# Optimization experiments

Hardware: AMD Instinct MI355X
Metric: run time of the kernel (lower is better)

## Reference

```python
import jax, jax.numpy as jnp
import numpy as np

B, L = 256, 50            # batch, n_pos (session length)
ITEM_DIM, POS_DIM = 128, 64
DIM = ITEM_DIM + POS_DIM  # 192
N_ITEMS = 50000
W = 20.0                  # temperature / init scale
LN_EPS = 1e-5


def renorm(t, max_norm=1.5):
    # torch Embedding max_norm semantics: clip row L2 norm to max_norm
    n = jnp.linalg.norm(t, axis=-1, keepdims=True)
    return t * jnp.minimum(1.0, max_norm / jnp.maximum(n, 1e-7))


def setup_inputs() -> dict:
    key = jax.random.key(0)
    ks = jax.random.split(key, 24)
    inv_w = 1.0 / W
    lb = 1.0 / np.sqrt(DIM)
    lb3 = 1.0 / np.sqrt(3 * DIM)
    u = lambda k, shape, b: jax.random.uniform(k, shape, jnp.float32, -b, b)
    emb = jax.random.normal(ks[0], (N_ITEMS, ITEM_DIM), jnp.float32).at[0].set(0.0)
    pos_emb = jax.random.normal(ks[1], (L + 1, POS_DIM), jnp.float32).at[0].set(0.0)
    return {
        'x': jax.random.randint(ks[20], (B, L), 0, N_ITEMS),
        'pos': jnp.sort(jax.random.randint(ks[21], (B, L), 1, L + 1), axis=-1),
        'emb': emb,
        'pos_emb': pos_emb,
        'vw0': jax.random.normal(ks[2], (1, DIM), jnp.float32) * inv_w,
        'vw1': jax.random.normal(ks[3], (DIM, DIM), jnp.float32) * inv_w,
        'vw2': jax.random.normal(ks[4], (DIM, DIM), jnp.float32) * inv_w,
        'vbias': jnp.zeros((DIM,), jnp.float32),
        'w1_W': u(ks[5], (DIM, DIM), lb), 'w1_b': u(ks[6], (DIM,), lb),
        'w2_W': u(ks[7], (DIM, DIM), lb), 'w2_b': u(ks[8], (DIM,), lb),
        'wA': jax.random.normal(ks[9], (1, L), jnp.float32) * inv_w,
        'wg1_W': u(ks[10], (DIM, DIM), lb), 'wg1_b': u(ks[11], (DIM,), lb),
        'wg2_W': u(ks[12], (DIM, DIM), lb), 'wg2_b': u(ks[13], (DIM,), lb),
        'gq': jax.random.normal(ks[14], (DIM, 1), jnp.float32) * inv_w,
        'wf_W': u(ks[15], (ITEM_DIM, 3 * DIM), lb3), 'wf_b': u(ks[16], (ITEM_DIM,), lb3),
        'ln_g': jnp.ones((DIM,), jnp.float32), 'ln_b': jnp.zeros((DIM,), jnp.float32),
    }


def reference(x, pos, emb, pos_emb, vw0, vw1, vw2, vbias, w1_W, w1_b, w2_W, w2_b,
              wA, wg1_W, wg1_b, wg2_W, wg2_b, gq, wf_W, wf_b, ln_g, ln_b):
    emb_r = renorm(emb)
    x_e = emb_r[x]                                   # [B,L,item_dim]
    p_e = renorm(pos_emb)[pos]                       # [B,L,pos_dim]
    x_ = jnp.concatenate([x_e, p_e], axis=-1)        # [B,L,D]
    mask = (x != 0)                                  # [B,L]

    # --- vanila (additive) attention, all n_pos targets in one fused pass ---
    K = x_ @ vw1                                     # [B,L,D]  (shared across targets)
    Q = x_ @ vw2                                     # [B,L,D]
    h = jax.nn.relu(K[:, None, :, :] + Q[:, :, None, :] + vbias)   # [B,Li,Lj,D]
    alpha = jnp.einsum('bijd,d->bij', h, vw0[0])     # scores over keys j
    alpha = jnp.where(mask[:, None, :], alpha, -jnp.inf)
    a = jax.nn.softmax(alpha, axis=-1)
    S = jnp.einsum('bij,bjd->bid', a, x_)            # [B,L,D]

    # --- MLP + LayerNorm + position mixing ---
    h2 = jax.nn.relu(S @ w1_W.T + w1_b)
    S2 = h2 @ w2_W.T + w2_b + S
    mu = jnp.mean(S2, axis=-1, keepdims=True)
    var = jnp.mean((S2 - mu) ** 2, axis=-1, keepdims=True)
    S3 = ln_g * (S2 - mu) * jax.lax.rsqrt(var + LN_EPS) + ln_b
    st = jnp.einsum('p,bpd->bd', wA[0], S3)[:, None, :]   # [B,1,D]

    # --- global attention ---
    sl = x_[:, -1:, :]                               # [B,1,D]
    g = jax.nn.sigmoid(x_ @ wg1_W.T + wg1_b + (sl @ wg2_W.T + wg2_b))
    ag = g @ gq                                      # [B,L,1]
    sg = jnp.einsum('blo,bld->bod', ag, x_)          # [B,1,D]

    # --- decoder: cosine-similarity logits against item embeddings ---
    c = jax.nn.selu(jnp.concatenate([st, sl, sg], axis=-1) @ wf_W.T + wf_b)[:, 0, :]
    c = c / jnp.linalg.norm(c, axis=-1, keepdims=True)
    le = emb_r[1:]
    le = le / jnp.linalg.norm(le, axis=-1, keepdims=True)
    z = W * (c @ le.T)                               # [B, n_items-1]
    return z
```

## Files before the change

### kernel.cpp

```cpp
#include <hip/hip_runtime.h>
#include <hip/hip_bf16.h>
#include <math.h>
#include <stdint.h>

#define BB 256
#define LL 50
#define IDIM 128
#define PDIM 64
#define DIM 192
#define NITEMS 50000
#define NOUT 49999
#define WSC 20.0f
#define EPS 1e-5f
#define WMAT (DIM * DIM)

typedef __attribute__((ext_vector_type(8))) short  short8;
typedef __attribute__((ext_vector_type(8))) unsigned short u16x8;
typedef __attribute__((ext_vector_type(4))) float  f32x4;

__device__ __forceinline__ unsigned short f2bf(float f) {
    unsigned int u = __float_as_uint(f);
    u = (u + 0x7FFFu + ((u >> 16) & 1u)) >> 16;
    return (unsigned short)u;
}
__device__ __forceinline__ float bf2f(unsigned short u) {
    unsigned int v = ((unsigned int)u) << 16;
    return __uint_as_float(v);
}
__device__ __forceinline__ short8 pack8(const float* v) {
    u16x8 o;
#pragma unroll
    for (int j = 0; j < 8; ++j) o[j] = f2bf(v[j]);
    return *(short8*)&o;
}

__global__ __launch_bounds__(256) void k_prep2(const float* __restrict__ emb,
                                               unsigned short* __restrict__ emb16,
                                               float* __restrict__ invn,
                                               const float* __restrict__ vw1, const float* __restrict__ vw2,
                                               const float* __restrict__ w1W, const float* __restrict__ w2W,
                                               const float* __restrict__ wg1W,
                                               unsigned short* __restrict__ Wout) {
    int blk = blockIdx.x;
    if (blk < 12500) {
        int row  = blk * 4 + (threadIdx.x >> 6);
        int lane = threadIdx.x & 63;
        const float* p = emb + (size_t)row * IDIM;
        float a = p[lane], b = p[lane + 64];
        emb16[(size_t)row * IDIM + lane]      = f2bf(a);
        emb16[(size_t)row * IDIM + lane + 64] = f2bf(b);
        float s = a * a + b * b;
#pragma unroll
        for (int off = 32; off; off >>= 1) s += __shfl_xor(s, off);
        if (lane == 0) {
            float n = sqrtf(s);
            invn[row] = (n > 0.f) ? 1.f / n : 0.f;
        }
    } else {
        int b = blk - 12500;
        int wi = b / 144;
        int pos = (b % 144) * 256 + threadIdx.x;
        int n = pos / DIM, k = pos - n * DIM;
        float v;
        if      (wi == 0) v = vw1[(size_t)k * DIM + n];
        else if (wi == 1) v = vw2[(size_t)k * DIM + n];
        else if (wi == 2) v = w1W[pos];
        else if (wi == 3) v = w2W[pos];
        else              v = wg1W[pos];
        Wout[(size_t)wi * WMAT + pos] = f2bf(v);
    }
}

__global__ __launch_bounds__(768, 3) void k_mega(
    const int* __restrict__ x, const int* __restrict__ pos,
    const float* __restrict__ emb, const float* __restrict__ pe,
    const unsigned short* __restrict__ W16,
    const float* __restrict__ vw0, const float* __restrict__ vbias,
    const float* __restrict__ w1b, const float* __restrict__ w2b,
    const float* __restrict__ wg1b, const float* __restrict__ wg2W,
    const float* __restrict__ wg2b, const float* __restrict__ gq,
    const float* __restrict__ wA, const float* __restrict__ lng,
    const float* __restrict__ lnb, const float* __restrict__ wfW,
    const float* __restrict__ wfb, unsigned short* __restrict__ Cb16g) {

    __shared__ unsigned short Bs16[64 * DIM];
    __shared__ unsigned short X16T[DIM * 72];
    __shared__ unsigned short Ab16[64 * 72];
    __shared__ float R1[LL * 196];
    __shared__ float R2[LL * 196];
    __shared__ float xlast[DIM];
    __shared__ float GLs[DIM];
    __shared__ float cvec[3 * DIM];
    __shared__ float stB[DIM], sgB[DIM];
    __shared__ float red2[6][128];
    __shared__ float ags[64];
    __shared__ int   msk[64];
    __shared__ float was[64];
    __shared__ float red[12];
    __shared__ int   xi[LL], pii[LL];

    const int b = blockIdx.x, t = threadIdx.x;
    const int wv = t >> 6, l = t & 63;
    const int lr = l & 15, lk = l >> 4;

    if (t < LL) {
        xi[t]  = x[b * LL + t];
        pii[t] = pos[b * LL + t];
    }
    if (t >= 64 && t < 128) ags[t - 64] = 0.f;
    if (t >= 128 && t < 128 + LL) was[t - 128] = wA[t - 128];
    __syncthreads();
    if (t < 64) msk[t] = (t < LL) ? xi[t] : 0;
    for (int r = wv; r < LL; r += 12) {
        float v0 = emb[(size_t)xi[r] * IDIM + l];
        float v1 = emb[(size_t)xi[r] * IDIM + l + 64];
        float v2 = pe[pii[r] * PDIM + l];
        float se = v0 * v0 + v1 * v1;
        float sp = v2 * v2;
#pragma unroll
        for (int off = 32; off; off >>= 1) {
            se += __shfl_xor(se, off);
            sp += __shfl_xor(sp, off);
        }
        float ne = sqrtf(se), np = sqrtf(sp);
        float sce = fminf(1.0f, 1.5f / fmaxf(ne, 1e-7f));
        float scp = fminf(1.0f, 1.5f / fmaxf(np, 1e-7f));
        v0 *= sce; v1 *= sce; v2 *= scp;
        int base = r * 384, sw = (r & 7) << 4;
        *(unsigned short*)((char*)Bs16 + ((base + l * 2) ^ sw))         = f2bf(v0);
        *(unsigned short*)((char*)Bs16 + ((base + (l + 64) * 2) ^ sw))  = f2bf(v1);
        *(unsigned short*)((char*)Bs16 + ((base + (l + 128) * 2) ^ sw)) = f2bf(v2);
        X16T[l * 72 + r]         = f2bf(v0);
        X16T[(l + 64) * 72 + r]  = f2bf(v1);
        X16T[(l + 128) * 72 + r] = f2bf(v2);
        if (r == 49) { xlast[l] = v0; xlast[l + 64] = v1; xlast[l + 128] = v2; }
    }
    for (int e = t; e < 14 * DIM; e += 768) Bs16[LL * DIM + e] = 0;
    for (int e = t; e < DIM * 14; e += 768) { int d = e / 14, j = 50 + (e - d * 14); X16T[d * 72 + j] = 0; }
    for (int e = t; e < 14 * 72; e += 768) Ab16[50 * 72 + e] = 0;
    __syncthreads();

    if (t < DIM) {
        float g = wg2b[t];
        const float* wr = wg2W + (size_t)t * DIM;
        float s0 = 0, s1 = 0, s2 = 0, s3 = 0;
        for (int k = 0; k < DIM; k += 4) {
            float4 w4 = *(const float4*)(wr + k);
            s0 += xlast[k] * w4.x; s1 += xlast[k + 1] * w4.y;
            s2 += xlast[k + 2] * w4.z; s3 += xlast[k + 3] * w4.w;
        }
        GLs[t] = g + ((s0 + s1) + (s2 + s3));
    }
    __syncthreads();

    for (int task = wv; task < 36; task += 12) {
        int out = task / 12, nt = task % 12;
        int ncol = nt * 16 + lr;
        const unsigned short* bp = W16 + (size_t)(out == 0 ? 0 : (out == 1 ? 1 : 4)) * WMAT
                                   + (size_t)ncol * DIM + lk * 8;
#pragma unroll
        for (int mt = 0; mt < 4; ++mt) {
            int row = mt * 16 + lr;
            f32x4 ac = {};
#pragma unroll
            for (int ks = 0; ks < 6; ++ks) {
                int byte = (row * 384 + (lk * 8 + ks * 32) * 2) ^ ((row & 7) << 4);
                short8 af = *(const short8*)((const char*)Bs16 + byte);
                short8 bf = *(const short8*)(bp + ks * 32);
                ac = __builtin_amdgcn_mfma_f32_16x16x32_bf16(af, bf, ac, 0, 0, 0);
            }
            if (out == 0) {
                float bia = vbias[ncol];
#pragma unroll
                for (int r = 0; r < 4; ++r) {
                    int gr = mt * 16 + lk * 4 + r;
                    if (gr < LL) R1[gr * 196 + ncol] = ac[r] + bia;
                }
            } else if (out == 1) {
#pragma unroll
                for (int r = 0; r < 4; ++r) {
                    int gr = mt * 16 + lk * 4 + r;
                    if (gr < LL) R2[gr * 196 + ncol] = ac[r];
                }
            } else {
                float bia = wg1b[ncol] + GLs[ncol];
                float gqv = gq[ncol];
                int gr0 = mt * 16 + lk * 4;
                float v0 = ac[0] + bia, v1 = ac[1] + bia, v2 = ac[2] + bia, v3 = ac[3] + bia;
                float c0 = (gr0 + 0 < LL) ? gqv / (1.f + expf(-v0)) : 0.f;
                float c1 = (gr0 + 1 < LL) ? gqv / (1.f + expf(-v1)) : 0.f;
                float c2 = (gr0 + 2 < LL) ? gqv / (1.f + expf(-v2)) : 0.f;
                float c3 = (gr0 + 3 < LL) ? gqv / (1.f + expf(-v3)) : 0.f;
#pragma unroll
                for (int off = 1; off < 16; off <<= 1) {
                    c0 += __shfl_xor(c0, off); c1 += __shfl_xor(c1, off);
                    c2 += __shfl_xor(c2, off); c3 += __shfl_xor(c3, off);
                }
                if (lr == 0) {
                    if (gr0 + 0 < LL) atomicAdd(&ags[gr0 + 0], c0);
                    if (gr0 + 1 < LL) atomicAdd(&ags[gr0 + 1], c1);
                    if (gr0 + 2 < LL) atomicAdd(&ags[gr0 + 2], c2);
                    if (gr0 + 3 < LL) atomicAdd(&ags[gr0 + 3], c3);
                }
            }
        }
    }
    __syncthreads();

    {
        const int d0 = wv * 16;
        float kr[16], wr[16];
        {
            const float* wp = vw0 + d0;
#pragma unroll
            for (int q = 0; q < 4; ++q) {
                float4 v = *(const float4*)(wp + q * 4);
                wr[q * 4] = v.x; wr[q * 4 + 1] = v.y; wr[q * 4 + 2] = v.z; wr[q * 4 + 3] = v.w;
            }
            if (l < LL) {
                const float* kp = R1 + l * 196 + d0;
#pragma unroll
                for (int q = 0; q < 4; ++q) {
                    float4 v = *(const float4*)(kp + q * 4);
                    kr[q * 4] = v.x; kr[q * 4 + 1] = v.y; kr[q * 4 + 2] = v.z; kr[q * 4 + 3] = v.w;
                }
            } else {
#pragma unroll
                for (int q = 0; q < 16; ++q) kr[q] = 0.f;
            }
        }
        __syncthreads();
        unsigned short* parts16 = (unsigned short*)R1;
        const float NEG = -__builtin_inff();
        bool valid = (l < LL) && (msk[l] != 0);
#pragma unroll
        for (int i0 = 0; i0 < LL; i0 += 25) {
            for (int i = 0; i < 25; ++i) {
                const float* qrow = R2 + (i0 + i) * 196 + d0;
                float b0 = 0, b1 = 0, b2 = 0, b3 = 0;
#pragma unroll
                for (int q = 0; q < 4; ++q) {
                    float4 qv = *(const float4*)(qrow + q * 4);
                    b0 += fmaxf(kr[q * 4 + 0] + qv.x, 0.f) * wr[q * 4 + 0];
                    b1 += fmaxf(kr[q * 4 + 1] + qv.y, 0.f) * wr[q * 4 + 1];
                    b2 += fmaxf(kr[q * 4 + 2] + qv.z, 0.f) * wr[q * 4 + 2];
                    b3 += fmaxf(kr[q * 4 + 3] + qv.w, 0.f) * wr[q * 4 + 3];
                }
                parts16[(wv * 25 + i) * 64 + l] = f2bf((b0 + b1) + (b2 + b3));
            }
            __syncthreads();
            for (int i = wv; i < 25; i += 12) {
                float aj = 0.f;
#pragma unroll
                for (int w2 = 0; w2 < 12; ++w2) aj += bf2f(parts16[(w2 * 25 + i) * 64 + l]);
                if (!valid) aj = NEG;
                float m = aj;
#pragma unroll
                for (int off = 32; off; off >>= 1) m = fmaxf(m, __shfl_xor(m, off));
                float e = valid ? expf(aj - m) : 0.f;
                float s = e;
#pragma unroll
                for (int off = 32; off; off >>= 1) s += __shfl_xor(s, off);
                Ab16[(i0 + i) * 72 + l] = f2bf(e / s);
            }
            __syncthreads();
        }
    }

    for (int task = wv; task < 48; task += 12) {
        int mt = task / 12, nt = task - (task / 12) * 12;
        int i0 = mt * 16, d0c = nt * 16;
        short8 aA0 = *(const short8*)(Ab16 + (i0 + lr) * 72 + lk * 8);
        short8 aA1 = *(const short8*)(Ab16 + (i0 + lr) * 72 + 32 + lk * 8);
        short8 bB0 = *(const short8*)(X16T + (d0c + lr) * 72 + lk * 8);
        short8 bB1 = *(const short8*)(X16T + (d0c + lr) * 72 + 32 + lk * 8);
        f32x4 ac = {};
        ac = __builtin_amdgcn_mfma_f32_16x16x32_bf16(aA0, bB0, ac, 0, 0, 0);
        ac = __builtin_amdgcn_mfma_f32_16x16x32_bf16(aA1, bB1, ac, 0, 0, 0);
        int d = d0c + lr;
#pragma unroll
        for (int r = 0; r < 4; ++r) {
            int i = i0 + lk * 4 + r;
            if (i < LL) {
                R2[i * 196 + d] = ac[r];
                int byte = (i * 384 + d * 2) ^ ((i & 7) << 4);
                *(unsigned short*)((char*)Bs16 + byte) = f2bf(ac[r]);
            }
        }
    }
    __syncthreads();

    {
        f32x4 h[4] = {};
        {
            int ncol = wv * 16 + lr;
            const unsigned short* bp = W16 + (size_t)2 * WMAT + (size_t)ncol * DIM + lk * 8;
#pragma unroll
            for (int mt = 0; mt < 4; ++mt) {
                int row = mt * 16 + lr;
#pragma unroll
                for (int ks = 0; ks < 6; ++ks) {
                    int byte = (row * 384 + (lk * 8 + ks * 32) * 2) ^ ((row & 7) << 4);
                    short8 sf = *(const short8*)((const char*)Bs16 + byte);
                    short8 bf = *(const short8*)(bp + ks * 32);
                    h[mt] = __builtin_amdgcn_mfma_f32_16x16x32_bf16(sf, bf, h[mt], 0, 0, 0);
                }
            }
        }
        __syncthreads();
        {
            int gc = wv * 16 + lr;
            float bia = w1b[gc];
#pragma unroll
            for (int mt = 0; mt < 4; ++mt)
#pragma unroll
                for (int r = 0; r < 4; ++r) {
                    int gr = mt * 16 + lk * 4 + r;
                    if (gr < LL) {
                        float v = fmaxf(h[mt][r] + bia, 0.f);
                        int byte = (gr * 384 + gc * 2) ^ ((gr & 7) << 4);
                        *(unsigned short*)((char*)Bs16 + byte) = f2bf(v);
                    }
                }
        }
    }
    __syncthreads();

    {
        int ncol = wv * 16 + lr;
        const unsigned short* bp = W16 + (size_t)3 * WMAT + (size_t)ncol * DIM + lk * 8;
        float bia = w2b[ncol];
#pragma unroll
        for (int mt = 0; mt < 4; ++mt) {
            int row = mt * 16 + lr;
            f32x4 ac = {};
#pragma unroll
            for (int ks = 0; ks < 6; ++ks) {
                int byte = (row * 384 + (lk * 8 + ks * 32) * 2) ^ ((row & 7) << 4);
                short8 hf = *(const short8*)((const char*)Bs16 + byte);
                short8 bf = *(const short8*)(bp + ks * 32);
                ac = __builtin_amdgcn_mfma_f32_16x16x32_bf16(hf, bf, ac, 0, 0, 0);
            }
#pragma unroll
            for (int r = 0; r < 4; ++r) {
                int gr = mt * 16 + lk * 4 + r;
                if (gr < LL) R2[gr * 196 + ncol] = ac[r] + bia + R2[gr * 196 + ncol];
            }
        }
    }
    __syncthreads();

    for (int r = wv; r < LL; r += 12) {
        float* p = R2 + r * 196;
        float v0 = p[l], v1 = p[l + 64], v2 = p[l + 128];
        float s = v0 + v1 + v2;
#pragma unroll
        for (int off = 32; off; off >>= 1) s += __shfl_xor(s, off);
        float mu = s * (1.f / DIM);
        float d0 = v0 - mu, d1 = v1 - mu, d2 = v2 - mu;
        float q = d0 * d0 + d1 * d1 + d2 * d2;
#pragma unroll
        for (int off = 32; off; off >>= 1) q += __shfl_xor(q, off);
        float inv = rsqrtf(q * (1.f / DIM) + EPS);
        p[l]       = lng[l] * d0 * inv + lnb[l];
        p[l + 64]  = lng[l + 64] * d1 * inv + lnb[l + 64];
        p[l + 128] = lng[l + 128] * d2 * inv + lnb[l + 128];
    }
    __syncthreads();

    if (t < DIM) {
        float st = 0.f;
        for (int p = 0; p < 25; ++p) st += was[p] * R2[p * 196 + t];
        cvec[t] = st;
        cvec[DIM + t] = xlast[t];
    } else if (t < 2 * DIM) {
        int d = t - DIM;
        float st = 0.f;
        for (int p = 25; p < LL; ++p) st += was[p] * R2[p * 196 + d];
        stB[d] = st;
    } else if (t < 3 * DIM) {
        int d = t - 2 * DIM;
        float sg = 0.f;
        const unsigned short* xr = X16T + d * 72;
        for (int p = 0; p < 25; ++p) sg += ags[p] * bf2f(xr[p]);
        cvec[2 * DIM + d] = sg;
    } else {
        int d = t - 3 * DIM;
        float sg = 0.f;
        const unsigned short* xr = X16T + d * 72;
        for (int p = 25; p < LL; ++p) sg += ags[p] * bf2f(xr[p]);
        sgB[d] = sg;
    }
    __syncthreads();
    if (t < DIM) {
        cvec[t] += stB[t];
        cvec[2 * DIM + t] += sgB[t];
    }
    __syncthreads();

    {
        int out = t & 127, part = t >> 7;
        float s = (part == 0) ? wfb[out] : 0.f;
        const float* wr = wfW + (size_t)out * (3 * DIM) + part * 96;
        const float* cv = cvec + part * 96;
        for (int e = 0; e < 96; e += 4) {
            float4 w4 = *(const float4*)(wr + e);
            s += cv[e] * w4.x + cv[e + 1] * w4.y + cv[e + 2] * w4.z + cv[e + 3] * w4.w;
        }
        red2[part][out] = s;
    }
    __syncthreads();
    float cj = 0.f;
    if (t < IDIM) {
        float s = red2[0][t] + red2[1][t] + red2[2][t]
                + red2[3][t] + red2[4][t] + red2[5][t];
        const float sa = 1.6732632423543772f, sc = 1.0507009873554805f;
        cj = sc * (s > 0.f ? s : sa * expm1f(s));
    }
    float sq = cj * cj;
#pragma unroll
    for (int off = 32; off; off >>= 1) sq += __shfl_xor(sq, off);
    if (l == 0 && wv < 2) red[wv] = sq;
    __syncthreads();
    if (t < IDIM) {
        float nrm = sqrtf(red[0] + red[1]);
        Cb16g[b * IDIM + t] = f2bf(cj / nrm);
    }
}

__global__ __launch_bounds__(256) void k_z7(const unsigned short* __restrict__ Cb16,
                                            const unsigned short* __restrict__ emb16,
                                            const float* __restrict__ invn,
                                            float* __restrict__ Z) {
    __shared__ float tr[4][64][36];
    int n0 = blockIdx.x * 64;
    int t = threadIdx.x, w = t >> 6, l = t & 63;
    int lr = l & 15, lk = l >> 4;

    short8 a[4][4];
#pragma unroll
    for (int mt = 0; mt < 4; ++mt) {
        int mrow = w * 64 + mt * 16 + lr;
        const unsigned short* ap = Cb16 + (size_t)mrow * IDIM + lk * 8;
#pragma unroll
        for (int ks = 0; ks < 4; ++ks) a[mt][ks] = *(const short8*)(ap + ks * 32);
    }
    bool tail = (n0 + 64) > NOUT;
    int q8 = l >> 3, s8 = l & 7;

#pragma unroll
    for (int g = 0; g < 2; ++g) {
        f32x4 acc[4][2] = {};
        float sc[2];
#pragma unroll
        for (int ntl = 0; ntl < 2; ++ntl) {
            int nt = g * 2 + ntl;
            int nrow = n0 + nt * 16 + lr;
            short8 bfr[4];
            if (nrow < NOUT) {
                const unsigned short* bp = emb16 + (size_t)(nrow + 1) * IDIM + lk * 8;
#pragma unroll
                for (int ks = 0; ks < 4; ++ks) bfr[ks] = *(const short8*)(bp + ks * 32);
                sc[ntl] = WSC * invn[nrow + 1];
            } else {
                short8 z = {};
#pragma unroll
                for (int ks = 0; ks < 4; ++ks) bfr[ks] = z;
                sc[ntl] = 0.f;
            }
#pragma unroll
            for (int mt = 0; mt < 4; ++mt)
#pragma unroll
                for (int ks = 0; ks < 4; ++ks)
                    acc[mt][ntl] = __builtin_amdgcn_mfma_f32_16x16x32_bf16(a[mt][ks], bfr[ks], acc[mt][ntl], 0, 0, 0);
        }
#pragma unroll
        for (int ntl = 0; ntl < 2; ++ntl)
#pragma unroll
            for (int mt = 0; mt < 4; ++mt)
#pragma unroll
                for (int r = 0; r < 4; ++r)
                    tr[w][mt * 16 + lk * 4 + r][ntl * 16 + lr] = acc[mt][ntl][r] * sc[ntl];
        __syncthreads();
#pragma unroll
        for (int it = 0; it < 8; ++it) {
            int row = it * 8 + q8;
            int gm  = w * 64 + row;
            float4 v = *(const float4*)&tr[w][row][s8 * 4];
            int c0 = n0 + g * 32 + s8 * 4;
            if (!tail) {
                *(float4*)&Z[(size_t)gm * NOUT + c0] = v;
            } else {
                float vv[4] = {v.x, v.y, v.z, v.w};
#pragma unroll
                for (int j = 0; j < 4; ++j)
                    if (c0 + j < NOUT) Z[(size_t)gm * NOUT + c0 + j] = vv[j];
            }
        }
        __syncthreads();
    }
}

extern "C" void kernel_launch(void* const* d_in, const int* in_sizes, int n_in,
                              void* d_out, int out_size, void* d_ws, size_t ws_size,
                              hipStream_t stream) {
    const int*   x     = (const int*)d_in[0];
    const int*   pos   = (const int*)d_in[1];
    const float* emb   = (const float*)d_in[2];
    const float* pose  = (const float*)d_in[3];
    const float* vw0   = (const float*)d_in[4];
    const float* vw1   = (const float*)d_in[5];
    const float* vw2   = (const float*)d_in[6];
    const float* vbias = (const float*)d_in[7];
    const float* w1W   = (const float*)d_in[8];
    const float* w1b   = (const float*)d_in[9];
    const float* w2W   = (const float*)d_in[10];
    const float* w2b   = (const float*)d_in[11];
    const float* wA    = (const float*)d_in[12];
    const float* wg1W  = (const float*)d_in[13];
    const float* wg1b  = (const float*)d_in[14];
    const float* wg2W  = (const float*)d_in[15];
    const float* wg2b  = (const float*)d_in[16];
    const float* gq    = (const float*)d_in[17];
    const float* wfW   = (const float*)d_in[18];
    const float* wfb   = (const float*)d_in[19];
    const float* lng   = (const float*)d_in[20];
    const float* lnb   = (const float*)d_in[21];
    float* Z = (float*)d_out;

    float* w = (float*)d_ws;
    float* invn = w; w += NITEMS;
    w = (float*)(((uintptr_t)w + 15) & ~(uintptr_t)15);
    unsigned short* emb16 = (unsigned short*)w; w += (size_t)NITEMS * IDIM / 2;
    unsigned short* W16   = (unsigned short*)w; w += (size_t)5 * WMAT / 2;
    unsigned short* Cb16  = (unsigned short*)w;

    k_prep2<<<12500 + 720, 256, 0, stream>>>(emb, emb16, invn,
                                             vw1, vw2, w1W, w2W, wg1W, W16);
    k_mega<<<BB, 768, 0, stream>>>(x, pos, emb, pose, W16,
                                   vw0, vbias, w1b, w2b, wg1b, wg2W, wg2b, gq,
                                   wA, lng, lnb, wfW, wfb, Cb16);
    k_z7<<<(NOUT + 63) / 64, 256, 0, stream>>>(Cb16, emb16, invn, Z);
}
```

Measured before the change: 102.6 us.

## Fold embedding bf16 conversion and norm computation into the mega kernel

The embedding-table conversion to bf16 and the inverse-norm computation move out of the prep kernel and into k_mega. Each of the 256 blocks converts 196 rows, split across two phases of its attention work, so the memory-bound conversion overlaps with the compute-heavy per-session work. The prep launch shrinks to only the weight transposes. The cost is that k_mega now does more global traffic and stays latency-limited. Coverage is exactly 256×196 = 50176 ≥ 50000 rows.

```diff
diff --git a/kernel.cpp b/kernel.cpp
--- a/kernel.cpp
+++ b/kernel.cpp
@@ -13,6 +13,7 @@
 #define WSC 20.0f
 #define EPS 1e-5f
 #define WMAT (DIM * DIM)
+#define ROWS_PER_BLK 196
 
 typedef __attribute__((ext_vector_type(8))) short  short8;
 typedef __attribute__((ext_vector_type(8))) unsigned short u16x8;
@@ -34,41 +35,21 @@
     return *(short8*)&o;
 }
 
-__global__ __launch_bounds__(256) void k_prep2(const float* __restrict__ emb,
-                                               unsigned short* __restrict__ emb16,
-                                               float* __restrict__ invn,
-                                               const float* __restrict__ vw1, const float* __restrict__ vw2,
+__global__ __launch_bounds__(256) void k_prepW(const float* __restrict__ vw1, const float* __restrict__ vw2,
                                                const float* __restrict__ w1W, const float* __restrict__ w2W,
                                                const float* __restrict__ wg1W,
                                                unsigned short* __restrict__ Wout) {
-    int blk = blockIdx.x;
-    if (blk < 12500) {
-        int row  = blk * 4 + (threadIdx.x >> 6);
-        int lane = threadIdx.x & 63;
-        const float* p = emb + (size_t)row * IDIM;
-        float a = p[lane], b = p[lane + 64];
-        emb16[(size_t)row * IDIM + lane]      = f2bf(a);
-        emb16[(size_t)row * IDIM + lane + 64] = f2bf(b);
-        float s = a * a + b * b;
-#pragma unroll
-        for (int off = 32; off; off >>= 1) s += __shfl_xor(s, off);
-        if (lane == 0) {
-            float n = sqrtf(s);
-            invn[row] = (n > 0.f) ? 1.f / n : 0.f;
-        }
-    } else {
-        int b = blk - 12500;
-        int wi = b / 144;
-        int pos = (b % 144) * 256 + threadIdx.x;
-        int n = pos / DIM, k = pos - n * DIM;
-        float v;
-        if      (wi == 0) v = vw1[(size_t)k * DIM + n];
-        else if (wi == 1) v = vw2[(size_t)k * DIM + n];
-        else if (wi == 2) v = w1W[pos];
-        else if (wi == 3) v = w2W[pos];
-        else              v = wg1W[pos];
-        Wout[(size_t)wi * WMAT + pos] = f2bf(v);
-    }
+    int b = blockIdx.x;
+    int wi = b / 144;
+    int pos = (b % 144) * 256 + threadIdx.x;
+    int n = pos / DIM, k = pos - n * DIM;
+    float v;
+    if      (wi == 0) v = vw1[(size_t)k * DIM + n];
+    else if (wi == 1) v = vw2[(size_t)k * DIM + n];
+    else if (wi == 2) v = w1W[pos];
+    else if (wi == 3) v = w2W[pos];
+    else              v = wg1W[pos];
+    Wout[(size_t)wi * WMAT + pos] = f2bf(v);
 }
 
 __global__ __launch_bounds__(768, 3) void k_mega(
@@ -81,7 +62,8 @@
     const float* __restrict__ wg2b, const float* __restrict__ gq,
     const float* __restrict__ wA, const float* __restrict__ lng,
     const float* __restrict__ lnb, const float* __restrict__ wfW,
-    const float* __restrict__ wfb, unsigned short* __restrict__ Cb16g) {
+    const float* __restrict__ wfb, unsigned short* __restrict__ Cb16g,
+    unsigned short* __restrict__ emb16, float* __restrict__ invn) {
 
     __shared__ unsigned short Bs16[64 * DIM];
     __shared__ unsigned short X16T[DIM * 72];
@@ -102,6 +84,7 @@
     const int b = blockIdx.x, t = threadIdx.x;
     const int wv = t >> 6, l = t & 63;
     const int lr = l & 15, lk = l >> 4;
+    const int cvt_base = b * ROWS_PER_BLK;
 
     if (t < LL) {
         xi[t]  = x[b * LL + t];
@@ -205,6 +188,21 @@
             }
         }
     }
+    for (int r = cvt_base + wv; r < cvt_base + 98; r += 12) {
+        if (r < NITEMS) {
+            float a = emb[(size_t)r * IDIM + l];
+            float c = emb[(size_t)r * IDIM + l + 64];
+            emb16[(size_t)r * IDIM + l]      = f2bf(a);
+            emb16[(size_t)r * IDIM + l + 64] = f2bf(c);
+            float s = a * a + c * c;
+#pragma unroll
+            for (int off = 32; off; off >>= 1) s += __shfl_xor(s, off);
+            if (l == 0) {
+                float n = sqrtf(s);
+                invn[r] = (n > 0.f) ? 1.f / n : 0.f;
+            }
+        }
+    }
     __syncthreads();
 
     {
@@ -285,6 +283,21 @@
                 R2[i * 196 + d] = ac[r];
                 int byte = (i * 384 + d * 2) ^ ((i & 7) << 4);
                 *(unsigned short*)((char*)Bs16 + byte) = f2bf(ac[r]);
+            }
+        }
+    }
+    for (int r = cvt_base + 98 + wv; r < cvt_base + ROWS_PER_BLK; r += 12) {
+        if (r < NITEMS) {
+            float a = emb[(size_t)r * IDIM + l];
+            float c = emb[(size_t)r * IDIM + l + 64];
+            emb16[(size_t)r * IDIM + l]      = f2bf(a);
+            emb16[(size_t)r * IDIM + l + 64] = f2bf(c);
+            float s = a * a + c * c;
+#pragma unroll
+            for (int off = 32; off; off >>= 1) s += __shfl_xor(s, off);
+            if (l == 0) {
+                float n = sqrtf(s);
+                invn[r] = (n > 0.f) ? 1.f / n : 0.f;
             }
         }
     }
@@ -535,10 +548,9 @@
     unsigned short* W16   = (unsigned short*)w; w += (size_t)5 * WMAT / 2;
     unsigned short* Cb16  = (unsigned short*)w;
 
-    k_prep2<<<12500 + 720, 256, 0, stream>>>(emb, emb16, invn,
-                                             vw1, vw2, w1W, w2W, wg1W, W16);
+    k_prepW<<<720, 256, 0, stream>>>(vw1, vw2, w1W, w2W, wg1W, W16);
     k_mega<<<BB, 768, 0, stream>>>(x, pos, emb, pose, W16,
                                    vw0, vbias, w1b, w2b, wg1b, wg2W, wg2b, gq,
-                                   wA, lng, lnb, wfW, wfb, Cb16);
+                                   wA, lng, lnb, wfW, wfb, Cb16, emb16, invn);
     k_z7<<<(NOUT + 63) / 64, 256, 0, stream>>>(Cb16, emb16, invn, Z);
 }
```

New measurement: 107.5 us. 1.05x slower.
